# Kernel tuning notes

Measured on AMD Instinct MI355X. Metric: run time of the kernel, lower is better.

The kernel has to match this reference:

```python
import jax, jax.numpy as jnp
import numpy as np

D = 9  # nodefeat_n1 = 3 (resnet feat) + 6 (pos)


def _lstm_scan(x, Wih, Whh, bih, bhh, reverse=False):
    # x: [T, B, D] -> hidden states [T, B, D]; torch gate order i,f,g,o
    B = x.shape[1]
    def step(carry, xt):
        h, c = carry
        g = xt @ Wih.T + bih + h @ Whh.T + bhh
        i = jax.nn.sigmoid(g[:, :D])
        f = jax.nn.sigmoid(g[:, D:2*D])
        gg = jnp.tanh(g[:, 2*D:3*D])
        o = jax.nn.sigmoid(g[:, 3*D:])
        c = f * c + i * gg
        h = o * jnp.tanh(c)
        return (h, c), h
    init = (jnp.zeros((B, D), x.dtype), jnp.zeros((B, D), x.dtype))
    _, hs = jax.lax.scan(step, init, x, reverse=reverse)
    return hs


def _forward(nodes_feature, pos, attmat, msg_W, msg_b, gru_Wih, gru_Whh, gru_bih, gru_bhh,
             ro1_W, ro1_b, ro2_W, ro2_b, lf_Wih, lf_Whh, lf_bih, lf_bhh,
             lb_Wih, lb_Whh, lb_bih, lb_bhh, lr1_W, lr1_b, lr2_W, lr2_b, num_rec):
    node_feat = jnp.concatenate([nodes_feature, pos], axis=-1)  # [N,T,M,D]
    N, T, M, _ = node_feat.shape
    # valid_node_num = num_rec[b, 0] in the original code
    valid = (jnp.arange(M)[None, :] < num_rec[:, 0:1]).astype(node_feat.dtype)  # [N,M]
    att = attmat * valid[:, None, None, :]  # zero out invalid source nodes q
    src = node_feat  # message sources (h_w)
    hv = node_feat   # GRU hidden (h_v)
    hidden = node_feat
    for _ in range(2):  # iterN = 2 message-passing rounds
        msg = src @ msg_W.T + msg_b                    # [N,T,M,D] message_fc
        m = jnp.einsum('btnq,btqd->btnd', att, msg)    # attention-weighted sum over q
        # single-step GRU cell (torch gate order r,z,n)
        gx = m @ gru_Wih.T + gru_bih
        gh = hv @ gru_Whh.T + gru_bhh
        r = jax.nn.sigmoid(gx[..., :D] + gh[..., :D])
        z = jax.nn.sigmoid(gx[..., D:2*D] + gh[..., D:2*D])
        n = jnp.tanh(gx[..., 2*D:] + r * gh[..., 2*D:])
        h_new = (1.0 - z) * n + z * hv
        hidden = h_new * valid[:, None, :, None]       # invalid nodes never updated -> stay zero
        src = hidden
        hv = hidden
    vmask = valid[:, None, :, None]
    # per-frame readout (pred_label0)
    p0 = jax.nn.relu(hidden @ ro1_W.T + ro1_b) @ ro2_W.T + ro2_b
    pred_label0 = p0 * vmask
    # bidirectional LSTM over time, batched over (batch, node)
    x = hidden.transpose(1, 0, 2, 3).reshape(T, N * M, D)  # [T, N*M, D]
    hf = _lstm_scan(x, lf_Wih, lf_Whh, lf_bih, lf_bhh, reverse=False)
    hb = _lstm_scan(x, lb_Wih, lb_Whh, lb_bih, lb_bhh, reverse=True)
    out = jnp.concatenate([hf, hb], axis=-1).reshape(T, N, M, 2 * D).transpose(1, 0, 2, 3)
    p = jax.nn.relu(out @ lr1_W.T + lr1_b) @ lr2_W.T + lr2_b
    pred_label = p * vmask
    return pred_label, pred_label0


def setup_inputs() -> dict:
    key = jax.random.key(0)
    ks = jax.random.split(key, 32)
    N, T, M = 8192, 20, 6
    def u(k, shape, fan_in):
        s = 1.0 / np.sqrt(fan_in).astype(np.float32)
        return jax.random.uniform(k, shape, jnp.float32, -s, s)
    return {
        "nodes_feature": jax.random.normal(ks[0], (N, T, M, 3), jnp.float32),
        "pos": jax.random.normal(ks[1], (N, T, M, 6), jnp.float32),
        "attmat": jax.random.uniform(ks[2], (N, T, M, M), jnp.float32),
        "msg_W": u(ks[3], (D, D), D), "msg_b": u(ks[4], (D,), D),
        "gru_Wih": u(ks[5], (3 * D, D), D), "gru_Whh": u(ks[6], (3 * D, D), D),
        "gru_bih": u(ks[7], (3 * D,), D), "gru_bhh": u(ks[8], (3 * D,), D),
        "ro1_W": u(ks[9], (D, D), D), "ro1_b": u(ks[10], (D,), D),
        "ro2_W": u(ks[11], (7, D), D), "ro2_b": u(ks[12], (7,), D),
        "lf_Wih": u(ks[13], (4 * D, D), D), "lf_Whh": u(ks[14], (4 * D, D), D),
        "lf_bih": u(ks[15], (4 * D,), D), "lf_bhh": u(ks[16], (4 * D,), D),
        "lb_Wih": u(ks[17], (4 * D, D), D), "lb_Whh": u(ks[18], (4 * D, D), D),
        "lb_bih": u(ks[19], (4 * D,), D), "lb_bhh": u(ks[20], (4 * D,), D),
        "lr1_W": u(ks[21], (D, 2 * D), 2 * D), "lr1_b": u(ks[22], (D,), 2 * D),
        "lr2_W": u(ks[23], (7, D), D), "lr2_b": u(ks[24], (7,), D),
        "num_rec": jax.random.randint(ks[25], (N, T), 1, M + 1),
    }


def reference(nodes_feature, pos, attmat, msg_W, msg_b, gru_Wih, gru_Whh, gru_bih, gru_bhh,
              ro1_W, ro1_b, ro2_W, ro2_b, lf_Wih, lf_Whh, lf_bih, lf_bhh,
              lb_Wih, lb_Whh, lb_bih, lb_bhh, lr1_W, lr1_b, lr2_W, lr2_b, num_rec):
    return _forward(nodes_feature, pos, attmat, msg_W, msg_b, gru_Wih, gru_Whh, gru_bih, gru_bhh,
                    ro1_W, ro1_b, ro2_W, ro2_b, lf_Wih, lf_Whh, lf_bih, lf_bhh,
                    lb_Wih, lb_Whh, lb_bih, lb_bhh, lr1_W, lr1_b, lr2_W, lr2_b, num_rec)
```

## Files before the change

### kernel.cpp

```cpp
#include <hip/hip_runtime.h>

#define N_    8192
#define T_    20
#define M_    6
#define D_    9
#define NM_   (N_*M_)
#define NMP_  (NM_/2)
#define NT_   (N_*T_)
#define NTM7_ (N_*T_*M_*7)

#define LOG2E 1.44269504088896f

typedef __attribute__((ext_vector_type(2))) float v2f;

__device__ __forceinline__ float sigm(float x){
    return __builtin_amdgcn_rcpf(1.f + __builtin_amdgcn_exp2f(-LOG2E * x));
}
__device__ __forceinline__ float tanh_(float x){
    return fmaf(2.f, __builtin_amdgcn_rcpf(1.f + __builtin_amdgcn_exp2f(-2.f*LOG2E * x)), -1.f);
}
__device__ __forceinline__ v2f splat(float s){ return (v2f){s, s}; }
__device__ __forceinline__ v2f sigm2(v2f x){ v2f r; r.x = sigm(x.x); r.y = sigm(x.y); return r; }
__device__ __forceinline__ v2f tanh2(v2f x){ v2f r; r.x = tanh_(x.x); r.y = tanh_(x.y); return r; }
__device__ __forceinline__ v2f relu2(v2f x){ v2f r; r.x = fmaxf(x.x,0.f); r.y = fmaxf(x.y,0.f); return r; }

__global__ __launch_bounds__(64) void k_gnn(
    const float* __restrict__ nf,
    const float* __restrict__ pos,
    const float* __restrict__ am,
    const float* __restrict__ msgW, const float* __restrict__ msgb,
    const float* __restrict__ gWih, const float* __restrict__ gWhh,
    const float* __restrict__ gbih, const float* __restrict__ gbhh,
    const float* __restrict__ ro1W, const float* __restrict__ ro1b,
    const float* __restrict__ ro2W, const float* __restrict__ ro2b,
    const int*   __restrict__ numrec,
    float* __restrict__ hid,
    float* __restrict__ out0)
{
    __shared__ v2f mbuf[11 * 58];

    const int lane = threadIdx.x & 63;
    const int g    = lane / 6;
    const int i    = lane - g * 6;
    const int gB   = g * 58;
    const bool lactive = (lane < 60);

    const int wbase = blockIdx.x * 20;
    const int ntA = lactive ? (wbase + g)      : 0;
    const int ntB = lactive ? (wbase + 10 + g) : 0;
    const int nA = ntA / T_, tA = ntA - nA * T_;
    const int nB = ntB / T_, tB = ntB - nB * T_;

    v2f s[D_];
    {
        const float* pA = nf + (size_t)ntA * 18 + i * 3;
        const float* pB = nf + (size_t)ntB * 18 + i * 3;
        #pragma unroll
        for (int k = 0; k < 3; ++k) { s[k].x = pA[k]; s[k].y = pB[k]; }
    }
    {
        const float2* pA = (const float2*)(pos + (size_t)ntA * 36 + i * 6);
        const float2* pB = (const float2*)(pos + (size_t)ntB * 36 + i * 6);
        #pragma unroll
        for (int k = 0; k < 3; ++k) {
            float2 a = pA[k], b = pB[k];
            s[3 + 2*k]     = (v2f){a.x, b.x};
            s[3 + 2*k + 1] = (v2f){a.y, b.y};
        }
    }
    v2f attr[M_];
    {
        const float2* pA = (const float2*)(am + (size_t)ntA * 36 + i * 6);
        const float2* pB = (const float2*)(am + (size_t)ntB * 36 + i * 6);
        #pragma unroll
        for (int k = 0; k < 3; ++k) {
            float2 a = pA[k], b = pB[k];
            attr[2*k]     = (v2f){a.x, b.x};
            attr[2*k + 1] = (v2f){a.y, b.y};
        }
    }
    const int nrA = numrec[nA * T_];
    const int nrB = numrec[nB * T_];
    #pragma unroll
    for (int q = 0; q < M_; ++q) {
        attr[q].x *= (q < nrA) ? 1.f : 0.f;
        attr[q].y *= (q < nrB) ? 1.f : 0.f;
    }
    v2f vmi; vmi.x = (i < nrA) ? 1.f : 0.f; vmi.y = (i < nrB) ? 1.f : 0.f;

    #pragma unroll
    for (int it = 0; it < 2; ++it) {
        #pragma unroll
        for (int d = 0; d < D_; ++d) {
            v2f a = splat(msgb[d]);
            #pragma unroll
            for (int k = 0; k < D_; ++k) a += s[k] * msgW[d*9 + k];
            mbuf[gB + d*6 + i] = a;
        }
        v2f mm[D_];
        #pragma unroll
        for (int d = 0; d < D_; ++d) {
            const float4* rp = (const float4*)&mbuf[gB + d*6];
            float4 p0 = rp[0], p1 = rp[1], p2 = rp[2];
            v2f a = attr[0] * (v2f){p0.x, p0.y};
            a += attr[1] * (v2f){p0.z, p0.w};
            a += attr[2] * (v2f){p1.x, p1.y};
            a += attr[3] * (v2f){p1.z, p1.w};
            a += attr[4] * (v2f){p2.x, p2.y};
            a += attr[5] * (v2f){p2.z, p2.w};
            mm[d] = a;
        }
        v2f grz[18], gxn[9], ghn[9];
        #pragma unroll
        for (int j = 0; j < 18; ++j) {
            v2f a = splat(gbih[j] + gbhh[j]);
            #pragma unroll
            for (int k = 0; k < D_; ++k) {
                a += mm[k] * gWih[j*9 + k];
                a += s[k]  * gWhh[j*9 + k];
            }
            grz[j] = a;
        }
        #pragma unroll
        for (int j = 0; j < 9; ++j) {
            v2f ax = splat(gbih[18 + j]), ah = splat(gbhh[18 + j]);
            #pragma unroll
            for (int k = 0; k < D_; ++k) {
                ax += mm[k] * gWih[(18 + j)*9 + k];
                ah += s[k]  * gWhh[(18 + j)*9 + k];
            }
            gxn[j] = ax; ghn[j] = ah;
        }
        #pragma unroll
        for (int d = 0; d < D_; ++d) {
            v2f r  = sigm2(grz[d]);
            v2f z  = sigm2(grz[9 + d]);
            v2f nn = tanh2(gxn[d] + r * ghn[d]);
            s[d] = vmi * ((splat(1.f) - z) * nn + z * s[d]);
        }
    }

    if (lactive) {
        float* hpA = hid + (size_t)(nA * M_ + i) * (T_ * D_) + tA * D_;
        float* hpB = hid + (size_t)(nB * M_ + i) * (T_ * D_) + tB * D_;
        #pragma unroll
        for (int d = 0; d < D_; ++d) { hpA[d] = s[d].x; hpB[d] = s[d].y; }
    }

    v2f q9[D_];
    #pragma unroll
    for (int d = 0; d < D_; ++d) {
        v2f a = splat(ro1b[d]);
        #pragma unroll
        for (int k = 0; k < D_; ++k) a += s[k] * ro1W[d*9 + k];
        q9[d] = relu2(a);
    }
    if (lactive) {
        float* opA = out0 + (size_t)ntA * 42 + i * 7;
        float* opB = out0 + (size_t)ntB * 42 + i * 7;
        #pragma unroll
        for (int j = 0; j < 7; ++j) {
            v2f a = splat(ro2b[j]);
            #pragma unroll
            for (int k = 0; k < D_; ++k) a += q9[k] * ro2W[j*9 + k];
            a *= vmi;
            opA[j] = a.x; opB[j] = a.y;
        }
    }
}

__global__ __launch_bounds__(64) void k_lstm(
    const float* __restrict__ hid,
    const float* __restrict__ fWih, const float* __restrict__ fWhh,
    const float* __restrict__ fbih, const float* __restrict__ fbhh,
    const float* __restrict__ bWih, const float* __restrict__ bWhh,
    const float* __restrict__ bbih, const float* __restrict__ bbhh,
    const float* __restrict__ lr1W, const float* __restrict__ lr1b,
    const float* __restrict__ lr2W, const float* __restrict__ lr2b,
    const int*   __restrict__ numrec,
    float* __restrict__ out)
{
    __shared__ float4 hxs4[8 * 11];
    __shared__ v2f    hstv[8 * 381];

    const int lane = threadIdx.x & 63;
    const int grp0 = lane / 9;
    const int d    = lane - grp0 * 9;
    const int row  = grp0;

    bool active = (grp0 < 7);
    int pi = blockIdx.x * 7 + (active ? grp0 : 0);
    active = active && (pi < NMP_);
    const int pair = active ? pi : 0;
    const int cA = pair * 2, cB = cA + 1;

    const float* xbA = hid + (size_t)cA * (T_ * D_);
    const float* xbB = hid + (size_t)cB * (T_ * D_);
    const int xrow = row * 11;
    const int hrow = row * 381;

    {
        float wxi[9], wxf[9], wxg[9], wxo[9], whi[9], whf[9], whg[9], who[9];
        #pragma unroll
        for (int k = 0; k < 9; ++k) {
            wxi[k] = fWih[(d     )*9 + k];  whi[k] = fWhh[(d     )*9 + k];
            wxf[k] = fWih[(9  + d)*9 + k];  whf[k] = fWhh[(9  + d)*9 + k];
            wxg[k] = fWih[(18 + d)*9 + k];  whg[k] = fWhh[(18 + d)*9 + k];
            wxo[k] = fWih[(27 + d)*9 + k];  who[k] = fWhh[(27 + d)*9 + k];
        }
        const float bi = fbih[d]      + fbhh[d];
        const float bf = fbih[9 + d]  + fbhh[9 + d];
        const float bg = fbih[18 + d] + fbhh[18 + d];
        const float bo = fbih[27 + d] + fbhh[27 + d];

        hxs4[xrow + d] = make_float4(0.f, 0.f, xbA[d], xbB[d]);
        v2f h = splat(0.f), c = splat(0.f);
        for (int t = 0; t < T_; ++t) {
            const float xnA = (t < T_-1) ? xbA[(t+1)*9 + d] : 0.f;
            const float xnB = (t < T_-1) ? xbB[(t+1)*9 + d] : 0.f;
            v2f gi = splat(bi), gf = splat(bf), gg = splat(bg), go = splat(bo);
            #pragma unroll
            for (int j = 0; j < 9; ++j) {
                float4 v = hxs4[xrow + j];
                v2f hj = (v2f){v.x, v.y}, xj = (v2f){v.z, v.w};
                gi += hj * whi[j]; gi += xj * wxi[j];
                gf += hj * whf[j]; gf += xj * wxf[j];
                gg += hj * whg[j]; gg += xj * wxg[j];
                go += hj * who[j]; go += xj * wxo[j];
            }
            c = sigm2(gf) * c + sigm2(gi) * tanh2(gg);
            h = sigm2(go) * tanh2(c);
            hstv[hrow + t*19 + d] = h;
            hxs4[xrow + d] = make_float4(h.x, h.y, xnA, xnB);
        }
    }

    {
        float wxi[9], wxf[9], wxg[9], wxo[9], whi[9], whf[9], whg[9], who[9];
        #pragma unroll
        for (int k = 0; k < 9; ++k) {
            wxi[k] = bWih[(d     )*9 + k];  whi[k] = bWhh[(d     )*9 + k];
            wxf[k] = bWih[(9  + d)*9 + k];  whf[k] = bWhh[(9  + d)*9 + k];
            wxg[k] = bWih[(18 + d)*9 + k];  whg[k] = bWhh[(18 + d)*9 + k];
            wxo[k] = bWih[(27 + d)*9 + k];  who[k] = bWhh[(27 + d)*9 + k];
        }
        const float bi = bbih[d]      + bbhh[d];
        const float bf = bbih[9 + d]  + bbhh[9 + d];
        const float bg = bbih[18 + d] + bbhh[18 + d];
        const float bo = bbih[27 + d] + bbhh[27 + d];

        hxs4[xrow + d] = make_float4(0.f, 0.f, xbA[19*9 + d], xbB[19*9 + d]);
        v2f h = splat(0.f), c = splat(0.f);
        for (int tt = T_ - 1; tt >= 0; --tt) {
            const float xnA = (tt > 0) ? xbA[(tt-1)*9 + d] : 0.f;
            const float xnB = (tt > 0) ? xbB[(tt-1)*9 + d] : 0.f;
            v2f gi = splat(bi), gf = splat(bf), gg = splat(bg), go = splat(bo);
            #pragma unroll
            for (int j = 0; j < 9; ++j) {
                float4 v = hxs4[xrow + j];
                v2f hj = (v2f){v.x, v.y}, xj = (v2f){v.z, v.w};
                gi += hj * whi[j]; gi += xj * wxi[j];
                gf += hj * whf[j]; gf += xj * wxf[j];
                gg += hj * whg[j]; gg += xj * wxg[j];
                go += hj * who[j]; go += xj * wxo[j];
            }
            c = sigm2(gf) * c + sigm2(gi) * tanh2(gg);
            h = sigm2(go) * tanh2(c);
            hstv[hrow + tt*19 + 9 + d] = h;
            hxs4[xrow + d] = make_float4(h.x, h.y, xnA, xnB);
        }
    }

    #pragma unroll 1
    for (int rr = 0; rr < 3; ++rr) {
        const int item = rr * 64 + lane;
        if (item >= 140) break;
        const int ch = item / 20;
        const int t  = item - ch * 20;
        const int pi2 = blockIdx.x * 7 + ch;
        if (pi2 >= NMP_) continue;
        const int base = ch * 381 + t * 19;

        v2f hf[9], hb[9];
        #pragma unroll
        for (int k = 0; k < 9; ++k) { hf[k] = hstv[base + k]; hb[k] = hstv[base + 9 + k]; }

        const int cA2 = pi2 * 2, cB2 = cA2 + 1;
        const int nA2 = cA2 / M_, mA2 = cA2 - nA2 * M_;
        const int nB2 = cB2 / M_, mB2 = cB2 - nB2 * M_;
        v2f vi;
        vi.x = (mA2 < numrec[nA2 * T_]) ? 1.f : 0.f;
        vi.y = (mB2 < numrec[nB2 * T_]) ? 1.f : 0.f;

        v2f q[9];
        #pragma unroll
        for (int dd = 0; dd < 9; ++dd) {
            v2f a = splat(lr1b[dd]);
            #pragma unroll
            for (int k = 0; k < 9; ++k) a += hf[k] * lr1W[dd*18 + k];
            #pragma unroll
            for (int k = 0; k < 9; ++k) a += hb[k] * lr1W[dd*18 + 9 + k];
            q[dd] = relu2(a);
        }
        float* opA = out + (size_t)((nA2 * T_ + t) * M_ + mA2) * 7;
        float* opB = out + (size_t)((nB2 * T_ + t) * M_ + mB2) * 7;
        #pragma unroll
        for (int j = 0; j < 7; ++j) {
            v2f a = splat(lr2b[j]);
            #pragma unroll
            for (int k = 0; k < 9; ++k) a += q[k] * lr2W[j*9 + k];
            a *= vi;
            opA[j] = a.x; opB[j] = a.y;
        }
    }
}

extern "C" void kernel_launch(void* const* d_in, const int* in_sizes, int n_in,
                              void* d_out, int out_size, void* d_ws, size_t ws_size,
                              hipStream_t stream) {
    const float* nf    = (const float*)d_in[0];
    const float* pos   = (const float*)d_in[1];
    const float* am    = (const float*)d_in[2];
    const float* msgW  = (const float*)d_in[3];
    const float* msgb  = (const float*)d_in[4];
    const float* gWih  = (const float*)d_in[5];
    const float* gWhh  = (const float*)d_in[6];
    const float* gbih  = (const float*)d_in[7];
    const float* gbhh  = (const float*)d_in[8];
    const float* ro1W  = (const float*)d_in[9];
    const float* ro1b  = (const float*)d_in[10];
    const float* ro2W  = (const float*)d_in[11];
    const float* ro2b  = (const float*)d_in[12];
    const float* lfWih = (const float*)d_in[13];
    const float* lfWhh = (const float*)d_in[14];
    const float* lfbih = (const float*)d_in[15];
    const float* lfbhh = (const float*)d_in[16];
    const float* lbWih = (const float*)d_in[17];
    const float* lbWhh = (const float*)d_in[18];
    const float* lbbih = (const float*)d_in[19];
    const float* lbbhh = (const float*)d_in[20];
    const float* lr1W  = (const float*)d_in[21];
    const float* lr1b  = (const float*)d_in[22];
    const float* lr2W  = (const float*)d_in[23];
    const float* lr2b  = (const float*)d_in[24];
    const int* numrec  = (const int*)d_in[25];

    float* hid = (float*)d_ws;

    float* outp = (float*)d_out;
    float* out0 = (float*)d_out + NTM7_;

    k_gnn <<<NT_ / 20, 64, 0, stream>>>(nf, pos, am, msgW, msgb, gWih, gWhh,
                                        gbih, gbhh, ro1W, ro1b, ro2W, ro2b,
                                        numrec, hid, out0);
    const int lgrid = (NMP_ + 6) / 7;
    k_lstm<<<lgrid, 64, 0, stream>>>(hid, lfWih, lfWhh, lfbih, lfbhh,
                                     lbWih, lbWhh, lbbih, lbbhh,
                                     lr1W, lr1b, lr2W, lr2b, numrec, outp);
}
```

Measured before the change: 283.2 us.

## Fuse LSTM readout into forward pass and run backward direction first

The backward LSTM now runs first and stores only its hidden states in shared memory. The forward LSTM then computes the two-layer readout per timestep inline, reusing the h values already loaded for the gate matmul, and writes outputs directly. The separate post-pass readout loop and the larger shared buffer for forward states are removed. In exchange the recurrent critical path gets extra per-step work and extra register pressure from the readout weights held per lane.

```diff
diff --git a/kernel.cpp b/kernel.cpp
--- a/kernel.cpp
+++ b/kernel.cpp
@@ -181,7 +181,8 @@
     float* __restrict__ out)
 {
     __shared__ float4 hxs4[8 * 11];
-    __shared__ v2f    hstv[8 * 381];
+    __shared__ v2f    hbv [8 * 181];
+    __shared__ v2f    qbuf[64];
 
     const int lane = threadIdx.x & 63;
     const int grp0 = lane / 9;
@@ -196,28 +197,46 @@
 
     const float* xbA = hid + (size_t)cA * (T_ * D_);
     const float* xbB = hid + (size_t)cB * (T_ * D_);
-    const int xrow = row * 11;
-    const int hrow = row * 381;
+    const int xrow  = row * 11;
+    const int hbrow = row * 181;
+    const int qrow  = row * 9;
+
+    const int nA2 = cA / M_, mA2 = cA - nA2 * M_;
+    const int nB2 = cB / M_, mB2 = cB - nB2 * M_;
+    v2f vi;
+    vi.x = (mA2 < numrec[nA2 * T_]) ? 1.f : 0.f;
+    vi.y = (mB2 < numrec[nB2 * T_]) ? 1.f : 0.f;
+    float* oA = out + (size_t)nA2 * (T_ * M_ * 7) + mA2 * 7;
+    float* oB = out + (size_t)nB2 * (T_ * M_ * 7) + mB2 * 7;
+
+    const int j7 = (d < 7) ? d : 0;
+    float w1[18], w2[9];
+    #pragma unroll
+    for (int k = 0; k < 18; ++k) w1[k] = lr1W[d * 18 + k];
+    #pragma unroll
+    for (int k = 0; k < 9; ++k)  w2[k] = lr2W[j7 * 9 + k];
+    const float b1 = lr1b[d];
+    const float b2 = lr2b[j7];
 
     {
         float wxi[9], wxf[9], wxg[9], wxo[9], whi[9], whf[9], whg[9], who[9];
         #pragma unroll
         for (int k = 0; k < 9; ++k) {
-            wxi[k] = fWih[(d     )*9 + k];  whi[k] = fWhh[(d     )*9 + k];
-            wxf[k] = fWih[(9  + d)*9 + k];  whf[k] = fWhh[(9  + d)*9 + k];
-            wxg[k] = fWih[(18 + d)*9 + k];  whg[k] = fWhh[(18 + d)*9 + k];
-            wxo[k] = fWih[(27 + d)*9 + k];  who[k] = fWhh[(27 + d)*9 + k];
-        }
-        const float bi = fbih[d]      + fbhh[d];
-        const float bf = fbih[9 + d]  + fbhh[9 + d];
-        const float bg = fbih[18 + d] + fbhh[18 + d];
-        const float bo = fbih[27 + d] + fbhh[27 + d];
-
-        hxs4[xrow + d] = make_float4(0.f, 0.f, xbA[d], xbB[d]);
+            wxi[k] = bWih[(d     )*9 + k];  whi[k] = bWhh[(d     )*9 + k];
+            wxf[k] = bWih[(9  + d)*9 + k];  whf[k] = bWhh[(9  + d)*9 + k];
+            wxg[k] = bWih[(18 + d)*9 + k];  whg[k] = bWhh[(18 + d)*9 + k];
+            wxo[k] = bWih[(27 + d)*9 + k];  who[k] = bWhh[(27 + d)*9 + k];
+        }
+        const float bi = bbih[d]      + bbhh[d];
+        const float bf = bbih[9 + d]  + bbhh[9 + d];
+        const float bg = bbih[18 + d] + bbhh[18 + d];
+        const float bo = bbih[27 + d] + bbhh[27 + d];
+
+        hxs4[xrow + d] = make_float4(0.f, 0.f, xbA[19*9 + d], xbB[19*9 + d]);
         v2f h = splat(0.f), c = splat(0.f);
-        for (int t = 0; t < T_; ++t) {
-            const float xnA = (t < T_-1) ? xbA[(t+1)*9 + d] : 0.f;
-            const float xnB = (t < T_-1) ? xbB[(t+1)*9 + d] : 0.f;
+        for (int tt = T_ - 1; tt >= 0; --tt) {
+            const float xnA = (tt > 0) ? xbA[(tt-1)*9 + d] : 0.f;
+            const float xnB = (tt > 0) ? xbB[(tt-1)*9 + d] : 0.f;
             v2f gi = splat(bi), gf = splat(bf), gg = splat(bg), go = splat(bo);
             #pragma unroll
             for (int j = 0; j < 9; ++j) {
@@ -230,7 +249,7 @@
             }
             c = sigm2(gf) * c + sigm2(gi) * tanh2(gg);
             h = sigm2(go) * tanh2(c);
-            hstv[hrow + t*19 + d] = h;
+            hbv[hbrow + tt*9 + d] = h;
             hxs4[xrow + d] = make_float4(h.x, h.y, xnA, xnB);
         }
     }
@@ -239,78 +258,82 @@
         float wxi[9], wxf[9], wxg[9], wxo[9], whi[9], whf[9], whg[9], who[9];
         #pragma unroll
         for (int k = 0; k < 9; ++k) {
-            wxi[k] = bWih[(d     )*9 + k];  whi[k] = bWhh[(d     )*9 + k];
-            wxf[k] = bWih[(9  + d)*9 + k];  whf[k] = bWhh[(9  + d)*9 + k];
-            wxg[k] = bWih[(18 + d)*9 + k];  whg[k] = bWhh[(18 + d)*9 + k];
-            wxo[k] = bWih[(27 + d)*9 + k];  who[k] = bWhh[(27 + d)*9 + k];
-        }
-        const float bi = bbih[d]      + bbhh[d];
-        const float bf = bbih[9 + d]  + bbhh[9 + d];
-        const float bg = bbih[18 + d] + bbhh[18 + d];
-        const float bo = bbih[27 + d] + bbhh[27 + d];
-
-        hxs4[xrow + d] = make_float4(0.f, 0.f, xbA[19*9 + d], xbB[19*9 + d]);
+            wxi[k] = fWih[(d     )*9 + k];  whi[k] = fWhh[(d     )*9 + k];
+            wxf[k] = fWih[(9  + d)*9 + k];  whf[k] = fWhh[(9  + d)*9 + k];
+            wxg[k] = fWih[(18 + d)*9 + k];  whg[k] = fWhh[(18 + d)*9 + k];
+            wxo[k] = fWih[(27 + d)*9 + k];  who[k] = fWhh[(27 + d)*9 + k];
+        }
+        const float bi = fbih[d]      + fbhh[d];
+        const float bf = fbih[9 + d]  + fbhh[9 + d];
+        const float bg = fbih[18 + d] + fbhh[18 + d];
+        const float bo = fbih[27 + d] + fbhh[27 + d];
+
+        hxs4[xrow + d] = make_float4(0.f, 0.f, xbA[d], xbB[d]);
         v2f h = splat(0.f), c = splat(0.f);
-        for (int tt = T_ - 1; tt >= 0; --tt) {
-            const float xnA = (tt > 0) ? xbA[(tt-1)*9 + d] : 0.f;
-            const float xnB = (tt > 0) ? xbB[(tt-1)*9 + d] : 0.f;
+        for (int t = 0; t < T_; ++t) {
+            const float xnA = (t < T_-1) ? xbA[(t+1)*9 + d] : 0.f;
+            const float xnB = (t < T_-1) ? xbB[(t+1)*9 + d] : 0.f;
+
+            v2f q = splat(b1);
+            if (t > 0) {
+                const int hb0 = hbrow + (t - 1) * 9;
+                #pragma unroll
+                for (int k = 0; k < 9; ++k) q += hbv[hb0 + k] * w1[9 + k];
+            }
+
             v2f gi = splat(bi), gf = splat(bf), gg = splat(bg), go = splat(bo);
+            v2f hjs[9];
             #pragma unroll
             for (int j = 0; j < 9; ++j) {
                 float4 v = hxs4[xrow + j];
                 v2f hj = (v2f){v.x, v.y}, xj = (v2f){v.z, v.w};
+                hjs[j] = hj;
                 gi += hj * whi[j]; gi += xj * wxi[j];
                 gf += hj * whf[j]; gf += xj * wxf[j];
                 gg += hj * whg[j]; gg += xj * wxg[j];
                 go += hj * who[j]; go += xj * wxo[j];
             }
+
+            if (t > 0) {
+                #pragma unroll
+                for (int k = 0; k < 9; ++k) q += hjs[k] * w1[k];
+                q = relu2(q);
+                qbuf[qrow + d] = q;
+                if (active && (d < 7)) {
+                    v2f a = splat(b2);
+                    #pragma unroll
+                    for (int k = 0; k < 9; ++k) a += qbuf[qrow + k] * w2[k];
+                    a *= vi;
+                    const int ot = (t - 1) * (M_ * 7);
+                    oA[ot + d] = a.x;  oB[ot + d] = a.y;
+                }
+            }
+
             c = sigm2(gf) * c + sigm2(gi) * tanh2(gg);
             h = sigm2(go) * tanh2(c);
-            hstv[hrow + tt*19 + 9 + d] = h;
             hxs4[xrow + d] = make_float4(h.x, h.y, xnA, xnB);
         }
-    }
-
-    #pragma unroll 1
-    for (int rr = 0; rr < 3; ++rr) {
-        const int item = rr * 64 + lane;
-        if (item >= 140) break;
-        const int ch = item / 20;
-        const int t  = item - ch * 20;
-        const int pi2 = blockIdx.x * 7 + ch;
-        if (pi2 >= NMP_) continue;
-        const int base = ch * 381 + t * 19;
-
-        v2f hf[9], hb[9];
-        #pragma unroll
-        for (int k = 0; k < 9; ++k) { hf[k] = hstv[base + k]; hb[k] = hstv[base + 9 + k]; }
-
-        const int cA2 = pi2 * 2, cB2 = cA2 + 1;
-        const int nA2 = cA2 / M_, mA2 = cA2 - nA2 * M_;
-        const int nB2 = cB2 / M_, mB2 = cB2 - nB2 * M_;
-        v2f vi;
-        vi.x = (mA2 < numrec[nA2 * T_]) ? 1.f : 0.f;
-        vi.y = (mB2 < numrec[nB2 * T_]) ? 1.f : 0.f;
-
-        v2f q[9];
-        #pragma unroll
-        for (int dd = 0; dd < 9; ++dd) {
-            v2f a = splat(lr1b[dd]);
-            #pragma unroll
-            for (int k = 0; k < 9; ++k) a += hf[k] * lr1W[dd*18 + k];
-            #pragma unroll
-            for (int k = 0; k < 9; ++k) a += hb[k] * lr1W[dd*18 + 9 + k];
-            q[dd] = relu2(a);
-        }
-        float* opA = out + (size_t)((nA2 * T_ + t) * M_ + mA2) * 7;
-        float* opB = out + (size_t)((nB2 * T_ + t) * M_ + mB2) * 7;
-        #pragma unroll
-        for (int j = 0; j < 7; ++j) {
-            v2f a = splat(lr2b[j]);
-            #pragma unroll
-            for (int k = 0; k < 9; ++k) a += q[k] * lr2W[j*9 + k];
-            a *= vi;
-            opA[j] = a.x; opB[j] = a.y;
+
+        {
+            v2f q = splat(b1);
+            const int hb0 = hbrow + 19 * 9;
+            #pragma unroll
+            for (int k = 0; k < 9; ++k) q += hbv[hb0 + k] * w1[9 + k];
+            #pragma unroll
+            for (int k = 0; k < 9; ++k) {
+                float4 v = hxs4[xrow + k];
+                q += (v2f){v.x, v.y} * w1[k];
+            }
+            q = relu2(q);
+            qbuf[qrow + d] = q;
+            if (active && (d < 7)) {
+                v2f a = splat(b2);
+                #pragma unroll
+                for (int k = 0; k < 9; ++k) a += qbuf[qrow + k] * w2[k];
+                a *= vi;
+                const int ot = 19 * (M_ * 7);
+                oA[ot + d] = a.x;  oB[ot + d] = a.y;
+            }
         }
     }
 }
```

New measurement: 303.7 us. 1.07x slower.

## Run forward and backward LSTM directions in separate wavefronts concurrently

Applied to the files above, without the earlier changes.

The LSTM kernel grows from one to two wavefronts per block, so the forward and backward recurrences run in parallel on separate waves with their own shared-memory state buffers instead of one after the other. A block barrier now precedes the readout, and the readout work is spread over 128 threads. This halves the serial latency of each block's recurrence, at the cost of more registers and LDS per block, which may reduce how many blocks fit per CU.

```diff
diff --git a/kernel.cpp b/kernel.cpp
--- a/kernel.cpp
+++ b/kernel.cpp
@@ -169,7 +169,7 @@
     }
 }
 
-__global__ __launch_bounds__(64) void k_lstm(
+__global__ __launch_bounds__(128) void k_lstm(
     const float* __restrict__ hid,
     const float* __restrict__ fWih, const float* __restrict__ fWhh,
     const float* __restrict__ fbih, const float* __restrict__ fbhh,
@@ -180,10 +180,12 @@
     const int*   __restrict__ numrec,
     float* __restrict__ out)
 {
-    __shared__ float4 hxs4[8 * 11];
-    __shared__ v2f    hstv[8 * 381];
-
-    const int lane = threadIdx.x & 63;
+    __shared__ float4 hxs4[2][8 * 11];
+    __shared__ v2f    hstv[7 * 381];
+
+    const int tid  = threadIdx.x;
+    const int wv   = tid >> 6;
+    const int lane = tid & 63;
     const int grp0 = lane / 9;
     const int d    = lane - grp0 * 9;
     const int row  = grp0;
@@ -196,10 +198,11 @@
 
     const float* xbA = hid + (size_t)cA * (T_ * D_);
     const float* xbB = hid + (size_t)cB * (T_ * D_);
-    const int xrow = row * 11;
-    const int hrow = row * 381;
-
-    {
+    const int  xrow   = row * 11;
+    const bool hwrite = (grp0 < 7);
+    const int  hrow   = hwrite ? row * 381 : 0;
+
+    if (wv == 0) {
         float wxi[9], wxf[9], wxg[9], wxo[9], whi[9], whf[9], whg[9], who[9];
         #pragma unroll
         for (int k = 0; k < 9; ++k) {
@@ -213,7 +216,7 @@
         const float bg = fbih[18 + d] + fbhh[18 + d];
         const float bo = fbih[27 + d] + fbhh[27 + d];
 
-        hxs4[xrow + d] = make_float4(0.f, 0.f, xbA[d], xbB[d]);
+        hxs4[0][xrow + d] = make_float4(0.f, 0.f, xbA[d], xbB[d]);
         v2f h = splat(0.f), c = splat(0.f);
         for (int t = 0; t < T_; ++t) {
             const float xnA = (t < T_-1) ? xbA[(t+1)*9 + d] : 0.f;
@@ -221,7 +224,7 @@
             v2f gi = splat(bi), gf = splat(bf), gg = splat(bg), go = splat(bo);
             #pragma unroll
             for (int j = 0; j < 9; ++j) {
-                float4 v = hxs4[xrow + j];
+                float4 v = hxs4[0][xrow + j];
                 v2f hj = (v2f){v.x, v.y}, xj = (v2f){v.z, v.w};
                 gi += hj * whi[j]; gi += xj * wxi[j];
                 gf += hj * whf[j]; gf += xj * wxf[j];
@@ -230,12 +233,10 @@
             }
             c = sigm2(gf) * c + sigm2(gi) * tanh2(gg);
             h = sigm2(go) * tanh2(c);
-            hstv[hrow + t*19 + d] = h;
-            hxs4[xrow + d] = make_float4(h.x, h.y, xnA, xnB);
-        }
-    }
-
-    {
+            if (hwrite) hstv[hrow + t*19 + d] = h;
+            hxs4[0][xrow + d] = make_float4(h.x, h.y, xnA, xnB);
+        }
+    } else {
         float wxi[9], wxf[9], wxg[9], wxo[9], whi[9], whf[9], whg[9], who[9];
         #pragma unroll
         for (int k = 0; k < 9; ++k) {
@@ -249,7 +250,7 @@
         const float bg = bbih[18 + d] + bbhh[18 + d];
         const float bo = bbih[27 + d] + bbhh[27 + d];
 
-        hxs4[xrow + d] = make_float4(0.f, 0.f, xbA[19*9 + d], xbB[19*9 + d]);
+        hxs4[1][xrow + d] = make_float4(0.f, 0.f, xbA[19*9 + d], xbB[19*9 + d]);
         v2f h = splat(0.f), c = splat(0.f);
         for (int tt = T_ - 1; tt >= 0; --tt) {
             const float xnA = (tt > 0) ? xbA[(tt-1)*9 + d] : 0.f;
@@ -257,7 +258,7 @@
             v2f gi = splat(bi), gf = splat(bf), gg = splat(bg), go = splat(bo);
             #pragma unroll
             for (int j = 0; j < 9; ++j) {
-                float4 v = hxs4[xrow + j];
+                float4 v = hxs4[1][xrow + j];
                 v2f hj = (v2f){v.x, v.y}, xj = (v2f){v.z, v.w};
                 gi += hj * whi[j]; gi += xj * wxi[j];
                 gf += hj * whf[j]; gf += xj * wxf[j];
@@ -266,14 +267,16 @@
             }
             c = sigm2(gf) * c + sigm2(gi) * tanh2(gg);
             h = sigm2(go) * tanh2(c);
-            hstv[hrow + tt*19 + 9 + d] = h;
-            hxs4[xrow + d] = make_float4(h.x, h.y, xnA, xnB);
-        }
-    }
+            if (hwrite) hstv[hrow + tt*19 + 9 + d] = h;
+            hxs4[1][xrow + d] = make_float4(h.x, h.y, xnA, xnB);
+        }
+    }
+
+    __syncthreads();
 
     #pragma unroll 1
-    for (int rr = 0; rr < 3; ++rr) {
-        const int item = rr * 64 + lane;
+    for (int rr = 0; rr < 2; ++rr) {
+        const int item = rr * 128 + tid;
         if (item >= 140) break;
         const int ch = item / 20;
         const int t  = item - ch * 20;
@@ -354,7 +357,7 @@
                                         gbih, gbhh, ro1W, ro1b, ro2W, ro2b,
                                         numrec, hid, out0);
     const int lgrid = (NMP_ + 6) / 7;
-    k_lstm<<<lgrid, 64, 0, stream>>>(hid, lfWih, lfWhh, lfbih, lfbhh,
-                                     lbWih, lbWhh, lbbih, lbbhh,
-                                     lr1W, lr1b, lr2W, lr2b, numrec, outp);
-}
+    k_lstm<<<lgrid, 128, 0, stream>>>(hid, lfWih, lfWhh, lfbih, lfbhh,
+                                      lbWih, lbWhh, lbbih, lbbhh,
+                                      lr1W, lr1b, lr2W, lr2b, numrec, outp);
+}
```

Result: faster. 274.4 us (-3.1%).

## Fuse GNN and bidirectional LSTM into one per-batch kernel via LDS

Applied to the files above, without the earlier changes.

Merges the GNN message-passing kernel and the LSTM kernel into a single kernel, with one 64-lane block per batch element covering all 20 frames and 6 nodes. GNN hidden states go to shared memory in a pair-interleaved layout instead of a global workspace, removing that round trip and a launch. The forward and backward LSTM directions now run concurrently on separate lane groups (3 node pairs × 2 directions) instead of sequentially. The price is two block barriers, more LDS per block, a launch-bounds occupancy hint, and a few idle lanes during the recurrence.

```diff
diff --git a/kernel.cpp b/kernel.cpp
--- a/kernel.cpp
+++ b/kernel.cpp
@@ -5,7 +5,6 @@
 #define M_    6
 #define D_    9
 #define NM_   (N_*M_)
-#define NMP_  (NM_/2)
 #define NT_   (N_*T_)
 #define NTM7_ (N_*T_*M_*7)
 
@@ -24,7 +23,7 @@
 __device__ __forceinline__ v2f tanh2(v2f x){ v2f r; r.x = tanh_(x.x); r.y = tanh_(x.y); return r; }
 __device__ __forceinline__ v2f relu2(v2f x){ v2f r; r.x = fmaxf(x.x,0.f); r.y = fmaxf(x.y,0.f); return r; }
 
-__global__ __launch_bounds__(64) void k_gnn(
+__global__ __launch_bounds__(64, 4) void k_fused(
     const float* __restrict__ nf,
     const float* __restrict__ pos,
     const float* __restrict__ am,
@@ -33,144 +32,6 @@
     const float* __restrict__ gbih, const float* __restrict__ gbhh,
     const float* __restrict__ ro1W, const float* __restrict__ ro1b,
     const float* __restrict__ ro2W, const float* __restrict__ ro2b,
-    const int*   __restrict__ numrec,
-    float* __restrict__ hid,
-    float* __restrict__ out0)
-{
-    __shared__ v2f mbuf[11 * 58];
-
-    const int lane = threadIdx.x & 63;
-    const int g    = lane / 6;
-    const int i    = lane - g * 6;
-    const int gB   = g * 58;
-    const bool lactive = (lane < 60);
-
-    const int wbase = blockIdx.x * 20;
-    const int ntA = lactive ? (wbase + g)      : 0;
-    const int ntB = lactive ? (wbase + 10 + g) : 0;
-    const int nA = ntA / T_, tA = ntA - nA * T_;
-    const int nB = ntB / T_, tB = ntB - nB * T_;
-
-    v2f s[D_];
-    {
-        const float* pA = nf + (size_t)ntA * 18 + i * 3;
-        const float* pB = nf + (size_t)ntB * 18 + i * 3;
-        #pragma unroll
-        for (int k = 0; k < 3; ++k) { s[k].x = pA[k]; s[k].y = pB[k]; }
-    }
-    {
-        const float2* pA = (const float2*)(pos + (size_t)ntA * 36 + i * 6);
-        const float2* pB = (const float2*)(pos + (size_t)ntB * 36 + i * 6);
-        #pragma unroll
-        for (int k = 0; k < 3; ++k) {
-            float2 a = pA[k], b = pB[k];
-            s[3 + 2*k]     = (v2f){a.x, b.x};
-            s[3 + 2*k + 1] = (v2f){a.y, b.y};
-        }
-    }
-    v2f attr[M_];
-    {
-        const float2* pA = (const float2*)(am + (size_t)ntA * 36 + i * 6);
-        const float2* pB = (const float2*)(am + (size_t)ntB * 36 + i * 6);
-        #pragma unroll
-        for (int k = 0; k < 3; ++k) {
-            float2 a = pA[k], b = pB[k];
-            attr[2*k]     = (v2f){a.x, b.x};
-            attr[2*k + 1] = (v2f){a.y, b.y};
-        }
-    }
-    const int nrA = numrec[nA * T_];
-    const int nrB = numrec[nB * T_];
-    #pragma unroll
-    for (int q = 0; q < M_; ++q) {
-        attr[q].x *= (q < nrA) ? 1.f : 0.f;
-        attr[q].y *= (q < nrB) ? 1.f : 0.f;
-    }
-    v2f vmi; vmi.x = (i < nrA) ? 1.f : 0.f; vmi.y = (i < nrB) ? 1.f : 0.f;
-
-    #pragma unroll
-    for (int it = 0; it < 2; ++it) {
-        #pragma unroll
-        for (int d = 0; d < D_; ++d) {
-            v2f a = splat(msgb[d]);
-            #pragma unroll
-            for (int k = 0; k < D_; ++k) a += s[k] * msgW[d*9 + k];
-            mbuf[gB + d*6 + i] = a;
-        }
-        v2f mm[D_];
-        #pragma unroll
-        for (int d = 0; d < D_; ++d) {
-            const float4* rp = (const float4*)&mbuf[gB + d*6];
-            float4 p0 = rp[0], p1 = rp[1], p2 = rp[2];
-            v2f a = attr[0] * (v2f){p0.x, p0.y};
-            a += attr[1] * (v2f){p0.z, p0.w};
-            a += attr[2] * (v2f){p1.x, p1.y};
-            a += attr[3] * (v2f){p1.z, p1.w};
-            a += attr[4] * (v2f){p2.x, p2.y};
-            a += attr[5] * (v2f){p2.z, p2.w};
-            mm[d] = a;
-        }
-        v2f grz[18], gxn[9], ghn[9];
-        #pragma unroll
-        for (int j = 0; j < 18; ++j) {
-            v2f a = splat(gbih[j] + gbhh[j]);
-            #pragma unroll
-            for (int k = 0; k < D_; ++k) {
-                a += mm[k] * gWih[j*9 + k];
-                a += s[k]  * gWhh[j*9 + k];
-            }
-            grz[j] = a;
-        }
-        #pragma unroll
-        for (int j = 0; j < 9; ++j) {
-            v2f ax = splat(gbih[18 + j]), ah = splat(gbhh[18 + j]);
-            #pragma unroll
-            for (int k = 0; k < D_; ++k) {
-                ax += mm[k] * gWih[(18 + j)*9 + k];
-                ah += s[k]  * gWhh[(18 + j)*9 + k];
-            }
-            gxn[j] = ax; ghn[j] = ah;
-        }
-        #pragma unroll
-        for (int d = 0; d < D_; ++d) {
-            v2f r  = sigm2(grz[d]);
-            v2f z  = sigm2(grz[9 + d]);
-            v2f nn = tanh2(gxn[d] + r * ghn[d]);
-            s[d] = vmi * ((splat(1.f) - z) * nn + z * s[d]);
-        }
-    }
-
-    if (lactive) {
-        float* hpA = hid + (size_t)(nA * M_ + i) * (T_ * D_) + tA * D_;
-        float* hpB = hid + (size_t)(nB * M_ + i) * (T_ * D_) + tB * D_;
-        #pragma unroll
-        for (int d = 0; d < D_; ++d) { hpA[d] = s[d].x; hpB[d] = s[d].y; }
-    }
-
-    v2f q9[D_];
-    #pragma unroll
-    for (int d = 0; d < D_; ++d) {
-        v2f a = splat(ro1b[d]);
-        #pragma unroll
-        for (int k = 0; k < D_; ++k) a += s[k] * ro1W[d*9 + k];
-        q9[d] = relu2(a);
-    }
-    if (lactive) {
-        float* opA = out0 + (size_t)ntA * 42 + i * 7;
-        float* opB = out0 + (size_t)ntB * 42 + i * 7;
-        #pragma unroll
-        for (int j = 0; j < 7; ++j) {
-            v2f a = splat(ro2b[j]);
-            #pragma unroll
-            for (int k = 0; k < D_; ++k) a += q9[k] * ro2W[j*9 + k];
-            a *= vmi;
-            opA[j] = a.x; opB[j] = a.y;
-        }
-    }
-}
-
-__global__ __launch_bounds__(64) void k_lstm(
-    const float* __restrict__ hid,
     const float* __restrict__ fWih, const float* __restrict__ fWhh,
     const float* __restrict__ fbih, const float* __restrict__ fbhh,
     const float* __restrict__ bWih, const float* __restrict__ bWhh,
@@ -178,46 +39,191 @@
     const float* __restrict__ lr1W, const float* __restrict__ lr1b,
     const float* __restrict__ lr2W, const float* __restrict__ lr2b,
     const int*   __restrict__ numrec,
-    float* __restrict__ out)
+    float* __restrict__ out,
+    float* __restrict__ out0)
 {
-    __shared__ float4 hxs4[8 * 11];
-    __shared__ v2f    hstv[8 * 381];
+    __shared__ float  hx[T_ * 3 * D_ * 2];
+    __shared__ float4 hxs4[7 * 11];
+    __shared__ v2f    shpool[1143];
 
     const int lane = threadIdx.x & 63;
-    const int grp0 = lane / 9;
-    const int d    = lane - grp0 * 9;
-    const int row  = grp0;
-
-    bool active = (grp0 < 7);
-    int pi = blockIdx.x * 7 + (active ? grp0 : 0);
-    active = active && (pi < NMP_);
-    const int pair = active ? pi : 0;
-    const int cA = pair * 2, cB = cA + 1;
-
-    const float* xbA = hid + (size_t)cA * (T_ * D_);
-    const float* xbB = hid + (size_t)cB * (T_ * D_);
-    const int xrow = row * 11;
-    const int hrow = row * 381;
+    const int n    = blockIdx.x;
 
     {
+        const int g    = lane / 6;
+        const int i    = lane - g * 6;
+        const int gB   = g * 58;
+        const bool lactive = (lane < 60);
+
+        const int wbase = n * 20;
+        const int ntA = lactive ? (wbase + g)      : wbase;
+        const int ntB = lactive ? (wbase + 10 + g) : wbase;
+        const int nA = ntA / T_, tA = ntA - nA * T_;
+        const int nB = ntB / T_, tB = ntB - nB * T_;
+
+        v2f s[D_];
+        {
+            const float* pA = nf + (size_t)ntA * 18 + i * 3;
+            const float* pB = nf + (size_t)ntB * 18 + i * 3;
+            #pragma unroll
+            for (int k = 0; k < 3; ++k) { s[k].x = pA[k]; s[k].y = pB[k]; }
+        }
+        {
+            const float2* pA = (const float2*)(pos + (size_t)ntA * 36 + i * 6);
+            const float2* pB = (const float2*)(pos + (size_t)ntB * 36 + i * 6);
+            #pragma unroll
+            for (int k = 0; k < 3; ++k) {
+                float2 a = pA[k], b = pB[k];
+                s[3 + 2*k]     = (v2f){a.x, b.x};
+                s[3 + 2*k + 1] = (v2f){a.y, b.y};
+            }
+        }
+        v2f attr[M_];
+        {
+            const float2* pA = (const float2*)(am + (size_t)ntA * 36 + i * 6);
+            const float2* pB = (const float2*)(am + (size_t)ntB * 36 + i * 6);
+            #pragma unroll
+            for (int k = 0; k < 3; ++k) {
+                float2 a = pA[k], b = pB[k];
+                attr[2*k]     = (v2f){a.x, b.x};
+                attr[2*k + 1] = (v2f){a.y, b.y};
+            }
+        }
+        const int nrA = numrec[nA * T_];
+        const int nrB = numrec[nB * T_];
+        #pragma unroll
+        for (int q = 0; q < M_; ++q) {
+            attr[q].x *= (q < nrA) ? 1.f : 0.f;
+            attr[q].y *= (q < nrB) ? 1.f : 0.f;
+        }
+        v2f vmi; vmi.x = (i < nrA) ? 1.f : 0.f; vmi.y = (i < nrB) ? 1.f : 0.f;
+
+        #pragma unroll
+        for (int it = 0; it < 2; ++it) {
+            #pragma unroll
+            for (int d = 0; d < D_; ++d) {
+                v2f a = splat(msgb[d]);
+                #pragma unroll
+                for (int k = 0; k < D_; ++k) a += s[k] * msgW[d*9 + k];
+                shpool[gB + d*6 + i] = a;
+            }
+            v2f mm[D_];
+            #pragma unroll
+            for (int d = 0; d < D_; ++d) {
+                const float4* rp = (const float4*)&shpool[gB + d*6];
+                float4 p0 = rp[0], p1 = rp[1], p2 = rp[2];
+                v2f a = attr[0] * (v2f){p0.x, p0.y};
+                a += attr[1] * (v2f){p0.z, p0.w};
+                a += attr[2] * (v2f){p1.x, p1.y};
+                a += attr[3] * (v2f){p1.z, p1.w};
+                a += attr[4] * (v2f){p2.x, p2.y};
+                a += attr[5] * (v2f){p2.z, p2.w};
+                mm[d] = a;
+            }
+            v2f grz[18], gxn[9], ghn[9];
+            #pragma unroll
+            for (int j = 0; j < 18; ++j) {
+                v2f a = splat(gbih[j] + gbhh[j]);
+                #pragma unroll
+                for (int k = 0; k < D_; ++k) {
+                    a += mm[k] * gWih[j*9 + k];
+                    a += s[k]  * gWhh[j*9 + k];
+                }
+                grz[j] = a;
+            }
+            #pragma unroll
+            for (int j = 0; j < 9; ++j) {
+                v2f ax = splat(gbih[18 + j]), ah = splat(gbhh[18 + j]);
+                #pragma unroll
+                for (int k = 0; k < D_; ++k) {
+                    ax += mm[k] * gWih[(18 + j)*9 + k];
+                    ah += s[k]  * gWhh[(18 + j)*9 + k];
+                }
+                gxn[j] = ax; ghn[j] = ah;
+            }
+            #pragma unroll
+            for (int d = 0; d < D_; ++d) {
+                v2f r  = sigm2(grz[d]);
+                v2f z  = sigm2(grz[9 + d]);
+                v2f nn = tanh2(gxn[d] + r * ghn[d]);
+                s[d] = vmi * ((splat(1.f) - z) * nn + z * s[d]);
+            }
+        }
+
+        if (lactive) {
+            const int pr = i >> 1, par = i & 1;
+            #pragma unroll
+            for (int d = 0; d < D_; ++d) {
+                hx[((tA*3 + pr)*9 + d)*2 + par] = s[d].x;
+                hx[((tB*3 + pr)*9 + d)*2 + par] = s[d].y;
+            }
+        }
+
+        v2f q9[D_];
+        #pragma unroll
+        for (int d = 0; d < D_; ++d) {
+            v2f a = splat(ro1b[d]);
+            #pragma unroll
+            for (int k = 0; k < D_; ++k) a += s[k] * ro1W[d*9 + k];
+            q9[d] = relu2(a);
+        }
+        if (lactive) {
+            float* opA = out0 + (size_t)ntA * 42 + i * 7;
+            float* opB = out0 + (size_t)ntB * 42 + i * 7;
+            #pragma unroll
+            for (int j = 0; j < 7; ++j) {
+                v2f a = splat(ro2b[j]);
+                #pragma unroll
+                for (int k = 0; k < D_; ++k) a += q9[k] * ro2W[j*9 + k];
+                a *= vmi;
+                opA[j] = a.x; opB[j] = a.y;
+            }
+        }
+    }
+
+    __syncthreads();
+
+    {
+        int grpL = lane / 9;
+        if (grpL == 7) grpL = 6;
+        const int dd  = (lane == 63) ? 0 : (lane - grpL * 9);
+        const bool sv   = (grpL < 6);
+        const int  p    = sv ? (grpL % 3) : 0;
+        const int  dir  = sv ? (grpL / 3) : 0;
+        const int  xrow = grpL * 11;
+
+        const float* Wih = dir ? bWih : fWih;
+        const float* Whh = dir ? bWhh : fWhh;
+        const float* Bih = dir ? bbih : fbih;
+        const float* Bhh = dir ? bbhh : fbhh;
+
         float wxi[9], wxf[9], wxg[9], wxo[9], whi[9], whf[9], whg[9], who[9];
         #pragma unroll
         for (int k = 0; k < 9; ++k) {
-            wxi[k] = fWih[(d     )*9 + k];  whi[k] = fWhh[(d     )*9 + k];
-            wxf[k] = fWih[(9  + d)*9 + k];  whf[k] = fWhh[(9  + d)*9 + k];
-            wxg[k] = fWih[(18 + d)*9 + k];  whg[k] = fWhh[(18 + d)*9 + k];
-            wxo[k] = fWih[(27 + d)*9 + k];  who[k] = fWhh[(27 + d)*9 + k];
-        }
-        const float bi = fbih[d]      + fbhh[d];
-        const float bf = fbih[9 + d]  + fbhh[9 + d];
-        const float bg = fbih[18 + d] + fbhh[18 + d];
-        const float bo = fbih[27 + d] + fbhh[27 + d];
-
-        hxs4[xrow + d] = make_float4(0.f, 0.f, xbA[d], xbB[d]);
+            wxi[k] = Wih[(dd     )*9 + k];  whi[k] = Whh[(dd     )*9 + k];
+            wxf[k] = Wih[(9  + dd)*9 + k];  whf[k] = Whh[(9  + dd)*9 + k];
+            wxg[k] = Wih[(18 + dd)*9 + k];  whg[k] = Whh[(18 + dd)*9 + k];
+            wxo[k] = Wih[(27 + dd)*9 + k];  who[k] = Whh[(27 + dd)*9 + k];
+        }
+        const float bi = Bih[dd]      + Bhh[dd];
+        const float bf = Bih[9 + dd]  + Bhh[9 + dd];
+        const float bg = Bih[18 + dd] + Bhh[18 + dd];
+        const float bo = Bih[27 + dd] + Bhh[27 + dd];
+
+        const int t0 = dir ? (T_ - 1) : 0;
+        const int ts = dir ? -1 : 1;
+        const int dir9 = dir * 9;
+
+        {
+            v2f x0 = *(const v2f*)&hx[((t0*3 + p)*9 + dd)*2];
+            hxs4[xrow + dd] = make_float4(0.f, 0.f, x0.x, x0.y);
+        }
         v2f h = splat(0.f), c = splat(0.f);
-        for (int t = 0; t < T_; ++t) {
-            const float xnA = (t < T_-1) ? xbA[(t+1)*9 + d] : 0.f;
-            const float xnB = (t < T_-1) ? xbB[(t+1)*9 + d] : 0.f;
+        for (int ss = 0; ss < T_; ++ss) {
+            const int t = t0 + ts * ss;
+            v2f xn = splat(0.f);
+            if (ss < T_ - 1) xn = *(const v2f*)&hx[(((t + ts)*3 + p)*9 + dd)*2];
+
             v2f gi = splat(bi), gf = splat(bf), gg = splat(bg), go = splat(bo);
             #pragma unroll
             for (int j = 0; j < 9; ++j) {
@@ -230,80 +236,40 @@
             }
             c = sigm2(gf) * c + sigm2(gi) * tanh2(gg);
             h = sigm2(go) * tanh2(c);
-            hstv[hrow + t*19 + d] = h;
-            hxs4[xrow + d] = make_float4(h.x, h.y, xnA, xnB);
+            if (sv) shpool[p*381 + t*19 + dir9 + dd] = h;
+            hxs4[xrow + dd] = make_float4(h.x, h.y, xn.x, xn.y);
         }
     }
 
-    {
-        float wxi[9], wxf[9], wxg[9], wxo[9], whi[9], whf[9], whg[9], who[9];
-        #pragma unroll
-        for (int k = 0; k < 9; ++k) {
-            wxi[k] = bWih[(d     )*9 + k];  whi[k] = bWhh[(d     )*9 + k];
-            wxf[k] = bWih[(9  + d)*9 + k];  whf[k] = bWhh[(9  + d)*9 + k];
-            wxg[k] = bWih[(18 + d)*9 + k];  whg[k] = bWhh[(18 + d)*9 + k];
-            wxo[k] = bWih[(27 + d)*9 + k];  who[k] = bWhh[(27 + d)*9 + k];
-        }
-        const float bi = bbih[d]      + bbhh[d];
-        const float bf = bbih[9 + d]  + bbhh[9 + d];
-        const float bg = bbih[18 + d] + bbhh[18 + d];
-        const float bo = bbih[27 + d] + bbhh[27 + d];
-
-        hxs4[xrow + d] = make_float4(0.f, 0.f, xbA[19*9 + d], xbB[19*9 + d]);
-        v2f h = splat(0.f), c = splat(0.f);
-        for (int tt = T_ - 1; tt >= 0; --tt) {
-            const float xnA = (tt > 0) ? xbA[(tt-1)*9 + d] : 0.f;
-            const float xnB = (tt > 0) ? xbB[(tt-1)*9 + d] : 0.f;
-            v2f gi = splat(bi), gf = splat(bf), gg = splat(bg), go = splat(bo);
-            #pragma unroll
-            for (int j = 0; j < 9; ++j) {
-                float4 v = hxs4[xrow + j];
-                v2f hj = (v2f){v.x, v.y}, xj = (v2f){v.z, v.w};
-                gi += hj * whi[j]; gi += xj * wxi[j];
-                gf += hj * whf[j]; gf += xj * wxf[j];
-                gg += hj * whg[j]; gg += xj * wxg[j];
-                go += hj * who[j]; go += xj * wxo[j];
-            }
-            c = sigm2(gf) * c + sigm2(gi) * tanh2(gg);
-            h = sigm2(go) * tanh2(c);
-            hstv[hrow + tt*19 + 9 + d] = h;
-            hxs4[xrow + d] = make_float4(h.x, h.y, xnA, xnB);
-        }
-    }
-
-    #pragma unroll 1
-    for (int rr = 0; rr < 3; ++rr) {
-        const int item = rr * 64 + lane;
-        if (item >= 140) break;
-        const int ch = item / 20;
-        const int t  = item - ch * 20;
-        const int pi2 = blockIdx.x * 7 + ch;
-        if (pi2 >= NMP_) continue;
-        const int base = ch * 381 + t * 19;
+    __syncthreads();
+
+    if (lane < 60) {
+        const int pp = lane / 20;
+        const int t  = lane - pp * 20;
+        const int base = pp * 381 + t * 19;
 
         v2f hf[9], hb[9];
         #pragma unroll
-        for (int k = 0; k < 9; ++k) { hf[k] = hstv[base + k]; hb[k] = hstv[base + 9 + k]; }
-
-        const int cA2 = pi2 * 2, cB2 = cA2 + 1;
-        const int nA2 = cA2 / M_, mA2 = cA2 - nA2 * M_;
-        const int nB2 = cB2 / M_, mB2 = cB2 - nB2 * M_;
+        for (int k = 0; k < 9; ++k) { hf[k] = shpool[base + k]; hb[k] = shpool[base + 9 + k]; }
+
+        const int mA2 = 2 * pp, mB2 = mA2 + 1;
+        const int nr = numrec[n * T_];
         v2f vi;
-        vi.x = (mA2 < numrec[nA2 * T_]) ? 1.f : 0.f;
-        vi.y = (mB2 < numrec[nB2 * T_]) ? 1.f : 0.f;
+        vi.x = (mA2 < nr) ? 1.f : 0.f;
+        vi.y = (mB2 < nr) ? 1.f : 0.f;
 
         v2f q[9];
         #pragma unroll
-        for (int dd = 0; dd < 9; ++dd) {
-            v2f a = splat(lr1b[dd]);
-            #pragma unroll
-            for (int k = 0; k < 9; ++k) a += hf[k] * lr1W[dd*18 + k];
-            #pragma unroll
-            for (int k = 0; k < 9; ++k) a += hb[k] * lr1W[dd*18 + 9 + k];
-            q[dd] = relu2(a);
-        }
-        float* opA = out + (size_t)((nA2 * T_ + t) * M_ + mA2) * 7;
-        float* opB = out + (size_t)((nB2 * T_ + t) * M_ + mB2) * 7;
+        for (int dd2 = 0; dd2 < 9; ++dd2) {
+            v2f a = splat(lr1b[dd2]);
+            #pragma unroll
+            for (int k = 0; k < 9; ++k) a += hf[k] * lr1W[dd2*18 + k];
+            #pragma unroll
+            for (int k = 0; k < 9; ++k) a += hb[k] * lr1W[dd2*18 + 9 + k];
+            q[dd2] = relu2(a);
+        }
+        float* opA = out + (size_t)((n * T_ + t) * M_ + mA2) * 7;
+        float* opB = out + (size_t)((n * T_ + t) * M_ + mB2) * 7;
         #pragma unroll
         for (int j = 0; j < 7; ++j) {
             v2f a = splat(lr2b[j]);
@@ -345,16 +311,13 @@
     const float* lr2b  = (const float*)d_in[24];
     const int* numrec  = (const int*)d_in[25];
 
-    float* hid = (float*)d_ws;
-
     float* outp = (float*)d_out;
     float* out0 = (float*)d_out + NTM7_;
 
-    k_gnn <<<NT_ / 20, 64, 0, stream>>>(nf, pos, am, msgW, msgb, gWih, gWhh,
-                                        gbih, gbhh, ro1W, ro1b, ro2W, ro2b,
-                                        numrec, hid, out0);
-    const int lgrid = (NMP_ + 6) / 7;
-    k_lstm<<<lgrid, 64, 0, stream>>>(hid, lfWih, lfWhh, lfbih, lfbhh,
-                                     lbWih, lbWhh, lbbih, lbbhh,
-                                     lr1W, lr1b, lr2W, lr2b, numrec, outp);
+    k_fused<<<N_, 64, 0, stream>>>(nf, pos, am, msgW, msgb, gWih, gWhh,
+                                   gbih, gbhh, ro1W, ro1b, ro2W, ro2b,
+                                   lfWih, lfWhh, lfbih, lfbhh,
+                                   lbWih, lbWhh, lbbih, lbbhh,
+                                   lr1W, lr1b, lr2W, lr2b, numrec,
+                                   outp, out0);
 }
```

Result: faster. 270.4 us (-4.5%).
